# Kernel optimization log

Measured on AMD Instinct MI355X. Metric: run time of the kernel, lower is better.

Reference implementation:

```python
import jax, jax.numpy as jnp
import numpy as np

N_NODES = 100000
N_EDGES = 1600000
IN_CH = 128
OUT_CH = 64


def setup_inputs() -> dict:
    key = jax.random.key(0)
    k1, k2, k3 = jax.random.split(key, 3)
    x = jax.random.normal(k1, (N_NODES, IN_CH), dtype=jnp.float32)
    edge_index = jax.random.randint(k2, (2, N_EDGES), 0, N_NODES, dtype=jnp.int64)
    # Glorot-style init for the GCN weight, zero bias (PyG defaults)
    W = jax.random.normal(k3, (IN_CH, OUT_CH), dtype=jnp.float32) * (1.0 / np.sqrt(IN_CH))
    b = jnp.zeros((OUT_CH,), dtype=jnp.float32)
    return {"x": x, "edge_index": edge_index, "W": W, "b": b}


def reference(x, edge_index, W, b):
    n = x.shape[0]
    # add self loops (GCNConv default add_self_loops=True)
    loop = jnp.arange(n, dtype=edge_index.dtype)
    row = jnp.concatenate([edge_index[0], loop])  # source
    col = jnp.concatenate([edge_index[1], loop])  # target
    # symmetric degree normalization on augmented graph
    deg = jax.ops.segment_sum(jnp.ones_like(col, dtype=x.dtype), col, num_segments=n)
    dinv = jnp.where(deg > 0, jax.lax.rsqrt(deg), 0.0)
    norm = dinv[row] * dinv[col]  # [E+N]
    # linear transform first (out_channels < in_channels), then gather-scale-scatter
    h = x @ W  # [N, OUT]
    msgs = h[row] * norm[:, None]  # [E+N, OUT]
    out = jax.ops.segment_sum(msgs, col, num_segments=n)  # [N, OUT]
    return out + b
```

## Files before the change

kernel.cpp:

```cpp
#include <hip/hip_runtime.h>
#include <hip/hip_bf16.h>


#define IN_CH 128
#define OUT_CH 64
#define BSHIFT 7
#define BNODES 128
#define MAX_NB 800
#define CH_EDGES 7168
#define SORT_CAP 4096
#define XSTR 136

typedef short bf16x8 __attribute__((ext_vector_type(8)));
typedef float f32x4  __attribute__((ext_vector_type(4)));

__device__ __forceinline__ unsigned short f2b(float f) {
    unsigned int u = __float_as_uint(f);
    return (unsigned short)((u + 0x7FFFu + ((u >> 16) & 1u)) >> 16);
}

__global__ __launch_bounds__(256) void wprep_kernel(const float* __restrict__ W,
                                                    unsigned short* __restrict__ wbt) {
    int t = blockIdx.x * 256 + threadIdx.x;
    int k = t >> 6, nn = t & 63;
    wbt[nn * IN_CH + k] = f2b(W[t]);
}

__global__ __launch_bounds__(1024) void count_kernel(const int* __restrict__ col,
                                                     int* __restrict__ blkcnt,
                                                     int E, int NBLK, int NB) {
    __shared__ int h[MAX_NB];
    int tid = threadIdx.x;
    for (int i = tid; i < NB; i += 1024) h[i] = 0;
    __syncthreads();
    int e0 = blockIdx.x * CH_EDGES;
    #pragma unroll
    for (int r = 0; r < CH_EDGES / 1024; ++r) {
        int e = e0 + r * 1024 + tid;
        if (e < E) atomicAdd(&h[col[e] >> BSHIFT], 1);
    }
    __syncthreads();
    for (int i = tid; i < NB; i += 1024) blkcnt[i * NBLK + blockIdx.x] = h[i];
}

__global__ __launch_bounds__(256) void scan1_kernel(const int* __restrict__ v_in,
                                                    int* __restrict__ partial, int n) {
    __shared__ int s[256];
    int tid = threadIdx.x;
    int i   = blockIdx.x * 256 + tid;
    int v   = (i < n) ? v_in[i] : 0;
    s[tid] = v; __syncthreads();
    #pragma unroll
    for (int off = 1; off < 256; off <<= 1) {
        int t = (tid >= off) ? s[tid - off] : 0;
        __syncthreads();
        s[tid] += t;
        __syncthreads();
    }
    if (tid == 255) partial[blockIdx.x] = s[255];
}

__global__ __launch_bounds__(1024) void scan2_kernel(int* __restrict__ partial, int nb) {
    __shared__ int s[1024];
    int tid = threadIdx.x;
    int v   = (tid < nb) ? partial[tid] : 0;
    s[tid] = v; __syncthreads();
    #pragma unroll
    for (int off = 1; off < 1024; off <<= 1) {
        int t = (tid >= off) ? s[tid - off] : 0;
        __syncthreads();
        s[tid] += t;
        __syncthreads();
    }
    if (tid < nb) partial[tid] = s[tid] - v;
}

__global__ __launch_bounds__(256) void scan3_kernel(const int* __restrict__ v_in,
                                                    const int* __restrict__ partial,
                                                    int* __restrict__ v_out,
                                                    int* __restrict__ bucket_start,
                                                    int n, int NBLK, int NB, int E) {
    __shared__ int s[256];
    int tid = threadIdx.x;
    int i   = blockIdx.x * 256 + tid;
    int v   = (i < n) ? v_in[i] : 0;
    s[tid] = v; __syncthreads();
    #pragma unroll
    for (int off = 1; off < 256; off <<= 1) {
        int t = (tid >= off) ? s[tid - off] : 0;
        __syncthreads();
        s[tid] += t;
        __syncthreads();
    }
    if (i < n) {
        int excl = partial[blockIdx.x] + s[tid] - v;
        v_out[i] = excl;
        if (i % NBLK == 0) bucket_start[i / NBLK] = excl;
    }
    if (i == 0) bucket_start[NB] = E;
}

__global__ __launch_bounds__(1024) void place_kernel(const int* __restrict__ row,
                                                     const int* __restrict__ col,
                                                     const int* __restrict__ blkoff,
                                                     int* __restrict__ pairs,
                                                     int E, int NBLK, int NB) {
    __shared__ int cur[MAX_NB];
    int tid = threadIdx.x;
    for (int i = tid; i < NB; i += 1024) cur[i] = blkoff[i * NBLK + blockIdx.x];
    __syncthreads();
    int e0 = blockIdx.x * CH_EDGES;
    #pragma unroll
    for (int r2 = 0; r2 < CH_EDGES / 1024; ++r2) {
        int e = e0 + r2 * 1024 + tid;
        if (e < E) {
            int c = col[e];
            int b = c >> BSHIFT;
            int pos = atomicAdd(&cur[b], 1);
            pairs[pos] = row[e] | ((c & (BNODES - 1)) << 17);
        }
    }
}

__global__ __launch_bounds__(256) void bucket_sort_kernel(
    const int* __restrict__ bucket_start, const int* __restrict__ pairs,
    int* __restrict__ csr_row, int* __restrict__ row_start,
    float* __restrict__ dinv, int n, int E)
{
    __shared__ int cnt[BNODES];
    __shared__ int deg[BNODES];
    __shared__ int cur[BNODES];
    __shared__ int sorted[SORT_CAP];

    int b = blockIdx.x, tid = threadIdx.x;
    int node0 = b << BSHIFT;
    int nodeCnt = min(BNODES, n - node0);
    int s0 = bucket_start[b], s1 = bucket_start[b + 1];
    int m = s1 - s0;

    if (tid < BNODES) cnt[tid] = 0;
    __syncthreads();
    for (int e = s0 + tid; e < s1; e += 256) atomicAdd(&cnt[pairs[e] >> 17], 1);
    __syncthreads();
    if (tid < BNODES) deg[tid] = cnt[tid];
    __syncthreads();
    #pragma unroll
    for (int off = 1; off < BNODES; off <<= 1) {
        int t = (tid >= off && tid < BNODES) ? cnt[tid - off] : 0;
        __syncthreads();
        if (tid < BNODES) cnt[tid] += t;
        __syncthreads();
    }
    if (tid < BNODES) {
        int excl = cnt[tid] - deg[tid];
        cur[tid] = excl;
        if (tid < nodeCnt) {
            row_start[node0 + tid] = s0 + excl;
            dinv[node0 + tid] = rsqrtf((float)(deg[tid] + 1));
        }
    }
    if (b == gridDim.x - 1 && tid == 0) row_start[n] = E;
    __syncthreads();

    if (m <= SORT_CAP) {
        for (int e = s0 + tid; e < s1; e += 256) {
            int p   = pairs[e];
            int pos = atomicAdd(&cur[p >> 17], 1);
            sorted[pos] = p & 0x1FFFF;
        }
        __syncthreads();
        for (int i = tid; i < m; i += 256) csr_row[s0 + i] = sorted[i];
    } else {
        if (tid < BNODES) cur[tid] += s0;
        __syncthreads();
        for (int e = s0 + tid; e < s1; e += 256) {
            int p   = pairs[e];
            int pos = atomicAdd(&cur[p >> 17], 1);
            csr_row[pos] = p & 0x1FFFF;
        }
    }
}

__global__ __launch_bounds__(256) void gemm_kernel(
    const float* __restrict__ x, const unsigned short* __restrict__ wbt,
    const float* __restrict__ dinv, unsigned short* __restrict__ hpb, int n)
{
    __shared__ __align__(16) unsigned short xl[64 * XSTR];
    __shared__ __align__(16) unsigned short wl[64 * XSTR];

    int tid  = threadIdx.x;
    int row0 = blockIdx.x * 64;

    {
        const uint4* src = (const uint4*)wbt;
        #pragma unroll
        for (int i = 0; i < 4; ++i) {
            int flat = tid + i * 256;
            int nn = flat >> 4, c = flat & 15;
            *(uint4*)(wl + nn * XSTR + c * 8) = src[flat];
        }
    }
    #pragma unroll
    for (int i = 0; i < 4; ++i) {
        int r  = (tid >> 4) + i * 16;
        int c  = tid & 15;
        int gr = row0 + r;
        float4 v0 = make_float4(0.f,0.f,0.f,0.f), v1 = v0;
        float d = 0.f;
        if (gr < n) {
            d = dinv[gr];
            const float4* xr = (const float4*)(x + (size_t)gr * IN_CH);
            v0 = xr[c * 2]; v1 = xr[c * 2 + 1];
        }
        uint4 p;
        p.x = ((unsigned)f2b(v0.y * d) << 16) | f2b(v0.x * d);
        p.y = ((unsigned)f2b(v0.w * d) << 16) | f2b(v0.z * d);
        p.z = ((unsigned)f2b(v1.y * d) << 16) | f2b(v1.x * d);
        p.w = ((unsigned)f2b(v1.w * d) << 16) | f2b(v1.z * d);
        *(uint4*)(xl + r * XSTR + c * 8) = p;
    }
    __syncthreads();

    int lane = tid & 63, w = tid >> 6;
    int mrow = lane & 15;
    int g    = lane >> 4;

    f32x4 acc0 = {0,0,0,0}, acc1 = {0,0,0,0}, acc2 = {0,0,0,0}, acc3 = {0,0,0,0};
    const unsigned short* xbase = xl + (w * 16 + mrow) * XSTR + g * 8;
    const unsigned short* wbase = wl + mrow * XSTR + g * 8;

    #pragma unroll
    for (int k4 = 0; k4 < 4; ++k4) {
        bf16x8 a  = *(const bf16x8*)(xbase + k4 * 32);
        bf16x8 b0 = *(const bf16x8*)(wbase +             k4 * 32);
        bf16x8 b1 = *(const bf16x8*)(wbase + 16 * XSTR + k4 * 32);
        bf16x8 b2 = *(const bf16x8*)(wbase + 32 * XSTR + k4 * 32);
        bf16x8 b3 = *(const bf16x8*)(wbase + 48 * XSTR + k4 * 32);
        acc0 = __builtin_amdgcn_mfma_f32_16x16x32_bf16(a, b0, acc0, 0, 0, 0);
        acc1 = __builtin_amdgcn_mfma_f32_16x16x32_bf16(a, b1, acc1, 0, 0, 0);
        acc2 = __builtin_amdgcn_mfma_f32_16x16x32_bf16(a, b2, acc2, 0, 0, 0);
        acc3 = __builtin_amdgcn_mfma_f32_16x16x32_bf16(a, b3, acc3, 0, 0, 0);
    }
    __syncthreads();

    {
        int cm = g * 4;
        #pragma unroll
        for (int r = 0; r < 4; ++r) {
            unsigned short* crow = xl + (w * 16 + cm + r) * XSTR + mrow;
            crow[ 0] = f2b(acc0[r]);
            crow[16] = f2b(acc1[r]);
            crow[32] = f2b(acc2[r]);
            crow[48] = f2b(acc3[r]);
        }
    }
    __syncthreads();
    #pragma unroll
    for (int i = 0; i < 2; ++i) {
        int flat = tid + i * 256;
        int r = flat >> 3, c = flat & 7;
        int gr = row0 + r;
        if (gr < n) {
            uint4 v = *(const uint4*)(xl + r * XSTR + c * 8);
            *(uint4*)(hpb + (size_t)gr * OUT_CH + c * 8) = v;
        }
    }
}

__global__ __launch_bounds__(256) void aggregate_kernel(
    const int* __restrict__ row_start, const int* __restrict__ csr_row,
    const unsigned short* __restrict__ hpb, const float* __restrict__ dinv,
    const float* __restrict__ bias, float* __restrict__ out, int n)
{
    int wid  = (blockIdx.x * 256 + threadIdx.x) >> 6;
    int lane = threadIdx.x & 63;
    if (wid >= n) return;
    int half = lane >> 5;
    int hl   = lane & 31;

    const unsigned int* hp32 = (const unsigned int*)hpb;

    int s0 = row_start[wid];
    int s1 = row_start[wid + 1];

    float a0l=0.f,a0h=0.f,a1l=0.f,a1h=0.f,a2l=0.f,a2h=0.f,a3l=0.f,a3h=0.f;

    for (int base = s0; base < s1; base += 64) {
        int cnt  = min(64, s1 - base);
        int ridx = (base + lane < s1) ? csr_row[base + lane] : 0;
        int j = 0;
        for (; j + 8 <= cnt; j += 8) {
            int r0 = __shfl(ridx, j     + half);
            int r1 = __shfl(ridx, j + 2 + half);
            int r2 = __shfl(ridx, j + 4 + half);
            int r3 = __shfl(ridx, j + 6 + half);
            unsigned int v0 = hp32[(size_t)r0 * 32 + hl];
            unsigned int v1 = hp32[(size_t)r1 * 32 + hl];
            unsigned int v2 = hp32[(size_t)r2 * 32 + hl];
            unsigned int v3 = hp32[(size_t)r3 * 32 + hl];
            a0l += __uint_as_float(v0 << 16); a0h += __uint_as_float(v0 & 0xFFFF0000u);
            a1l += __uint_as_float(v1 << 16); a1h += __uint_as_float(v1 & 0xFFFF0000u);
            a2l += __uint_as_float(v2 << 16); a2h += __uint_as_float(v2 & 0xFFFF0000u);
            a3l += __uint_as_float(v3 << 16); a3h += __uint_as_float(v3 & 0xFFFF0000u);
        }
        for (; j < cnt; j += 2) {
            int e = j + half;
            int r = __shfl(ridx, e);
            unsigned int v = (e < cnt) ? hp32[(size_t)r * 32 + hl] : 0u;
            a0l += __uint_as_float(v << 16); a0h += __uint_as_float(v & 0xFFFF0000u);
        }
    }
    float sl = ((a0l + a1l) + (a2l + a3l));
    float sh = ((a0h + a1h) + (a2h + a3h));
    sl += __shfl_xor(sl, 32);
    sh += __shfl_xor(sh, 32);

    if (half == 0) {
        unsigned int sv = hp32[(size_t)wid * 32 + hl];
        sl += __uint_as_float(sv << 16);
        sh += __uint_as_float(sv & 0xFFFF0000u);
        float d = dinv[wid];
        float2 bb = ((const float2*)bias)[hl];
        float2 o;
        o.x = fmaf(d, sl, bb.x);
        o.y = fmaf(d, sh, bb.y);
        ((float2*)(out + (size_t)wid * OUT_CH))[hl] = o;
    }
}

extern "C" void kernel_launch(void* const* d_in, const int* in_sizes, int n_in,
                              void* d_out, int out_size, void* d_ws, size_t ws_size,
                              hipStream_t stream) {
    const float* x  = (const float*)d_in[0];
    const int*   ei = (const int*)d_in[1];
    const float* W  = (const float*)d_in[2];
    const float* b  = (const float*)d_in[3];
    float*       out = (float*)d_out;

    int n = in_sizes[0] / IN_CH;
    int E = in_sizes[1] / 2;
    const int* row = ei;
    const int* col = ei + E;

    int NB   = (n + BNODES - 1) >> BSHIFT;
    int NBLK = (E + CH_EDGES - 1) / CH_EDGES;
    int TOT  = NB * NBLK;
    int nbs  = (TOT + 255) / 256;

    char* ws = (char*)d_ws;
    int*   blkcnt       = (int*)ws;   ws += (size_t)TOT * 4;
    int*   blkoff       = (int*)ws;   ws += (size_t)TOT * 4;
    int*   partial      = (int*)ws;   ws += 1024 * 4;
    int*   bucket_start = (int*)ws;   ws += (size_t)(NB + 1) * 4;
    int*   row_start    = (int*)ws;   ws += (size_t)(n + 1) * 4;
    float* dinv         = (float*)ws; ws += (size_t)n * 4;
    int*   csr_row      = (int*)ws;   ws += (size_t)E * 4;
    unsigned short* wbt = (unsigned short*)ws; ws += (size_t)IN_CH * OUT_CH * 2;
    ws = (char*)(((uintptr_t)ws + 255) & ~(uintptr_t)255);
    int*            pairs = (int*)ws;
    unsigned short* hpb   = (unsigned short*)ws;

    wprep_kernel      <<<(IN_CH * OUT_CH) / 256, 256, 0, stream>>>(W, wbt);
    count_kernel      <<<NBLK, 1024, 0, stream>>>(col, blkcnt, E, NBLK, NB);
    scan1_kernel      <<<nbs, 256, 0, stream>>>(blkcnt, partial, TOT);
    scan2_kernel      <<<1, 1024, 0, stream>>>(partial, nbs);
    scan3_kernel      <<<nbs, 256, 0, stream>>>(blkcnt, partial, blkoff, bucket_start,
                                                TOT, NBLK, NB, E);
    place_kernel      <<<NBLK, 1024, 0, stream>>>(row, col, blkoff, pairs, E, NBLK, NB);
    bucket_sort_kernel<<<NB, 256, 0, stream>>>(bucket_start, pairs, csr_row, row_start, dinv, n, E);
    gemm_kernel       <<<(n + 63) / 64, 256, 0, stream>>>(x, wbt, dinv, hpb, n);
    aggregate_kernel  <<<(n + 3) / 4, 256, 0, stream>>>(row_start, csr_row, hpb, dinv, b, out, n);
}
```

Before: 185.9 us.

## Replace per-block count scan with global bucket atomics; widen aggregate unroll

Each count block now adds its local histogram straight into global per-bucket totals. A single-block scan then produces bucket starts and cursors, and place recounts its chunk locally before reserving ranges with one global atomic per bucket. This drops the blkcnt matrix and two scan kernels, trading them for a recount of col in place and a nondeterministic edge order within each bucket, which bucket_sort later sorts. The aggregate inner loop also moves to 16 edges per iteration with 8 independent accumulator pairs and predicated tails, for more memory-level parallelism.

```diff
diff --git a/kernel.cpp b/kernel.cpp
--- a/kernel.cpp
+++ b/kernel.cpp
@@ -20,15 +20,18 @@
 }
 
 __global__ __launch_bounds__(256) void wprep_kernel(const float* __restrict__ W,
-                                                    unsigned short* __restrict__ wbt) {
+                                                    unsigned short* __restrict__ wbt,
+                                                    int* __restrict__ bucket_cnt,
+                                                    int NB) {
     int t = blockIdx.x * 256 + threadIdx.x;
     int k = t >> 6, nn = t & 63;
     wbt[nn * IN_CH + k] = f2b(W[t]);
+    if (t < NB) bucket_cnt[t] = 0;
 }
 
 __global__ __launch_bounds__(1024) void count_kernel(const int* __restrict__ col,
-                                                     int* __restrict__ blkcnt,
-                                                     int E, int NBLK, int NB) {
+                                                     int* __restrict__ bucket_cnt,
+                                                     int E, int NB) {
     __shared__ int h[MAX_NB];
     int tid = threadIdx.x;
     for (int i = tid; i < NB; i += 1024) h[i] = 0;
@@ -40,30 +43,17 @@
         if (e < E) atomicAdd(&h[col[e] >> BSHIFT], 1);
     }
     __syncthreads();
-    for (int i = tid; i < NB; i += 1024) blkcnt[i * NBLK + blockIdx.x] = h[i];
-}
-
-__global__ __launch_bounds__(256) void scan1_kernel(const int* __restrict__ v_in,
-                                                    int* __restrict__ partial, int n) {
-    __shared__ int s[256];
-    int tid = threadIdx.x;
-    int i   = blockIdx.x * 256 + tid;
-    int v   = (i < n) ? v_in[i] : 0;
-    s[tid] = v; __syncthreads();
-    #pragma unroll
-    for (int off = 1; off < 256; off <<= 1) {
-        int t = (tid >= off) ? s[tid - off] : 0;
-        __syncthreads();
-        s[tid] += t;
-        __syncthreads();
-    }
-    if (tid == 255) partial[blockIdx.x] = s[255];
-}
-
-__global__ __launch_bounds__(1024) void scan2_kernel(int* __restrict__ partial, int nb) {
+    for (int i = tid; i < NB; i += 1024)
+        if (h[i]) atomicAdd(&bucket_cnt[i], h[i]);
+}
+
+__global__ __launch_bounds__(1024) void scanB_kernel(const int* __restrict__ bucket_cnt,
+                                                     int* __restrict__ bucket_start,
+                                                     int* __restrict__ cursor,
+                                                     int NB, int E) {
     __shared__ int s[1024];
     int tid = threadIdx.x;
-    int v   = (tid < nb) ? partial[tid] : 0;
+    int v   = (tid < NB) ? bucket_cnt[tid] : 0;
     s[tid] = v; __syncthreads();
     #pragma unroll
     for (int off = 1; off < 1024; off <<= 1) {
@@ -72,51 +62,42 @@
         s[tid] += t;
         __syncthreads();
     }
-    if (tid < nb) partial[tid] = s[tid] - v;
-}
-
-__global__ __launch_bounds__(256) void scan3_kernel(const int* __restrict__ v_in,
-                                                    const int* __restrict__ partial,
-                                                    int* __restrict__ v_out,
-                                                    int* __restrict__ bucket_start,
-                                                    int n, int NBLK, int NB, int E) {
-    __shared__ int s[256];
-    int tid = threadIdx.x;
-    int i   = blockIdx.x * 256 + tid;
-    int v   = (i < n) ? v_in[i] : 0;
-    s[tid] = v; __syncthreads();
-    #pragma unroll
-    for (int off = 1; off < 256; off <<= 1) {
-        int t = (tid >= off) ? s[tid - off] : 0;
-        __syncthreads();
-        s[tid] += t;
-        __syncthreads();
-    }
-    if (i < n) {
-        int excl = partial[blockIdx.x] + s[tid] - v;
-        v_out[i] = excl;
-        if (i % NBLK == 0) bucket_start[i / NBLK] = excl;
-    }
-    if (i == 0) bucket_start[NB] = E;
+    if (tid < NB) {
+        int excl = s[tid] - v;
+        bucket_start[tid] = excl;
+        cursor[tid] = excl;
+    }
+    if (tid == 0) bucket_start[NB] = E;
 }
 
 __global__ __launch_bounds__(1024) void place_kernel(const int* __restrict__ row,
                                                      const int* __restrict__ col,
-                                                     const int* __restrict__ blkoff,
+                                                     int* __restrict__ cursor,
                                                      int* __restrict__ pairs,
-                                                     int E, int NBLK, int NB) {
-    __shared__ int cur[MAX_NB];
+                                                     int E, int NB) {
+    __shared__ int h[MAX_NB];
     int tid = threadIdx.x;
-    for (int i = tid; i < NB; i += 1024) cur[i] = blkoff[i * NBLK + blockIdx.x];
+    for (int i = tid; i < NB; i += 1024) h[i] = 0;
     __syncthreads();
     int e0 = blockIdx.x * CH_EDGES;
+    #pragma unroll
+    for (int r1 = 0; r1 < CH_EDGES / 1024; ++r1) {
+        int e = e0 + r1 * 1024 + tid;
+        if (e < E) atomicAdd(&h[col[e] >> BSHIFT], 1);
+    }
+    __syncthreads();
+    for (int i = tid; i < NB; i += 1024) {
+        int c = h[i];
+        if (c) h[i] = atomicAdd(&cursor[i], c);
+    }
+    __syncthreads();
     #pragma unroll
     for (int r2 = 0; r2 < CH_EDGES / 1024; ++r2) {
         int e = e0 + r2 * 1024 + tid;
         if (e < E) {
             int c = col[e];
             int b = c >> BSHIFT;
-            int pos = atomicAdd(&cur[b], 1);
+            int pos = atomicAdd(&h[b], 1);
             pairs[pos] = row[e] | ((c & (BNODES - 1)) << 17);
         }
     }
@@ -283,35 +264,41 @@
     int s0 = row_start[wid];
     int s1 = row_start[wid + 1];
 
-    float a0l=0.f,a0h=0.f,a1l=0.f,a1h=0.f,a2l=0.f,a2h=0.f,a3l=0.f,a3h=0.f;
+    float al0=0.f,al1=0.f,al2=0.f,al3=0.f,al4=0.f,al5=0.f,al6=0.f,al7=0.f;
+    float ah0=0.f,ah1=0.f,ah2=0.f,ah3=0.f,ah4=0.f,ah5=0.f,ah6=0.f,ah7=0.f;
 
     for (int base = s0; base < s1; base += 64) {
         int cnt  = min(64, s1 - base);
         int ridx = (base + lane < s1) ? csr_row[base + lane] : 0;
-        int j = 0;
-        for (; j + 8 <= cnt; j += 8) {
-            int r0 = __shfl(ridx, j     + half);
-            int r1 = __shfl(ridx, j + 2 + half);
-            int r2 = __shfl(ridx, j + 4 + half);
-            int r3 = __shfl(ridx, j + 6 + half);
-            unsigned int v0 = hp32[(size_t)r0 * 32 + hl];
-            unsigned int v1 = hp32[(size_t)r1 * 32 + hl];
-            unsigned int v2 = hp32[(size_t)r2 * 32 + hl];
-            unsigned int v3 = hp32[(size_t)r3 * 32 + hl];
-            a0l += __uint_as_float(v0 << 16); a0h += __uint_as_float(v0 & 0xFFFF0000u);
-            a1l += __uint_as_float(v1 << 16); a1h += __uint_as_float(v1 & 0xFFFF0000u);
-            a2l += __uint_as_float(v2 << 16); a2h += __uint_as_float(v2 & 0xFFFF0000u);
-            a3l += __uint_as_float(v3 << 16); a3h += __uint_as_float(v3 & 0xFFFF0000u);
-        }
-        for (; j < cnt; j += 2) {
-            int e = j + half;
-            int r = __shfl(ridx, e);
-            unsigned int v = (e < cnt) ? hp32[(size_t)r * 32 + hl] : 0u;
-            a0l += __uint_as_float(v << 16); a0h += __uint_as_float(v & 0xFFFF0000u);
-        }
-    }
-    float sl = ((a0l + a1l) + (a2l + a3l));
-    float sh = ((a0h + a1h) + (a2h + a3h));
+        for (int j0 = 0; j0 < cnt; j0 += 16) {
+            int e0 = j0      + half, e1 = j0 +  2 + half;
+            int e2 = j0 +  4 + half, e3 = j0 +  6 + half;
+            int e4 = j0 +  8 + half, e5 = j0 + 10 + half;
+            int e6 = j0 + 12 + half, e7 = j0 + 14 + half;
+            int r0 = __shfl(ridx, e0), r1 = __shfl(ridx, e1);
+            int r2 = __shfl(ridx, e2), r3 = __shfl(ridx, e3);
+            int r4 = __shfl(ridx, e4), r5 = __shfl(ridx, e5);
+            int r6 = __shfl(ridx, e6), r7 = __shfl(ridx, e7);
+            unsigned v0 = (e0 < cnt) ? hp32[(size_t)r0 * 32 + hl] : 0u;
+            unsigned v1 = (e1 < cnt) ? hp32[(size_t)r1 * 32 + hl] : 0u;
+            unsigned v2 = (e2 < cnt) ? hp32[(size_t)r2 * 32 + hl] : 0u;
+            unsigned v3 = (e3 < cnt) ? hp32[(size_t)r3 * 32 + hl] : 0u;
+            unsigned v4 = (e4 < cnt) ? hp32[(size_t)r4 * 32 + hl] : 0u;
+            unsigned v5 = (e5 < cnt) ? hp32[(size_t)r5 * 32 + hl] : 0u;
+            unsigned v6 = (e6 < cnt) ? hp32[(size_t)r6 * 32 + hl] : 0u;
+            unsigned v7 = (e7 < cnt) ? hp32[(size_t)r7 * 32 + hl] : 0u;
+            al0 += __uint_as_float(v0 << 16); ah0 += __uint_as_float(v0 & 0xFFFF0000u);
+            al1 += __uint_as_float(v1 << 16); ah1 += __uint_as_float(v1 & 0xFFFF0000u);
+            al2 += __uint_as_float(v2 << 16); ah2 += __uint_as_float(v2 & 0xFFFF0000u);
+            al3 += __uint_as_float(v3 << 16); ah3 += __uint_as_float(v3 & 0xFFFF0000u);
+            al4 += __uint_as_float(v4 << 16); ah4 += __uint_as_float(v4 & 0xFFFF0000u);
+            al5 += __uint_as_float(v5 << 16); ah5 += __uint_as_float(v5 & 0xFFFF0000u);
+            al6 += __uint_as_float(v6 << 16); ah6 += __uint_as_float(v6 & 0xFFFF0000u);
+            al7 += __uint_as_float(v7 << 16); ah7 += __uint_as_float(v7 & 0xFFFF0000u);
+        }
+    }
+    float sl = ((al0 + al1) + (al2 + al3)) + ((al4 + al5) + (al6 + al7));
+    float sh = ((ah0 + ah1) + (ah2 + ah3)) + ((ah4 + ah5) + (ah6 + ah7));
     sl += __shfl_xor(sl, 32);
     sh += __shfl_xor(sh, 32);
 
@@ -344,14 +331,11 @@
 
     int NB   = (n + BNODES - 1) >> BSHIFT;
     int NBLK = (E + CH_EDGES - 1) / CH_EDGES;
-    int TOT  = NB * NBLK;
-    int nbs  = (TOT + 255) / 256;
 
     char* ws = (char*)d_ws;
-    int*   blkcnt       = (int*)ws;   ws += (size_t)TOT * 4;
-    int*   blkoff       = (int*)ws;   ws += (size_t)TOT * 4;
-    int*   partial      = (int*)ws;   ws += 1024 * 4;
+    int*   bucket_cnt   = (int*)ws;   ws += (size_t)NB * 4;
     int*   bucket_start = (int*)ws;   ws += (size_t)(NB + 1) * 4;
+    int*   cursor       = (int*)ws;   ws += (size_t)NB * 4;
     int*   row_start    = (int*)ws;   ws += (size_t)(n + 1) * 4;
     float* dinv         = (float*)ws; ws += (size_t)n * 4;
     int*   csr_row      = (int*)ws;   ws += (size_t)E * 4;
@@ -360,13 +344,10 @@
     int*            pairs = (int*)ws;
     unsigned short* hpb   = (unsigned short*)ws;
 
-    wprep_kernel      <<<(IN_CH * OUT_CH) / 256, 256, 0, stream>>>(W, wbt);
-    count_kernel      <<<NBLK, 1024, 0, stream>>>(col, blkcnt, E, NBLK, NB);
-    scan1_kernel      <<<nbs, 256, 0, stream>>>(blkcnt, partial, TOT);
-    scan2_kernel      <<<1, 1024, 0, stream>>>(partial, nbs);
-    scan3_kernel      <<<nbs, 256, 0, stream>>>(blkcnt, partial, blkoff, bucket_start,
-                                                TOT, NBLK, NB, E);
-    place_kernel      <<<NBLK, 1024, 0, stream>>>(row, col, blkoff, pairs, E, NBLK, NB);
+    wprep_kernel      <<<(IN_CH * OUT_CH) / 256, 256, 0, stream>>>(W, wbt, bucket_cnt, NB);
+    count_kernel      <<<NBLK, 1024, 0, stream>>>(col, bucket_cnt, E, NB);
+    scanB_kernel      <<<1, 1024, 0, stream>>>(bucket_cnt, bucket_start, cursor, NB, E);
+    place_kernel      <<<NBLK, 1024, 0, stream>>>(row, col, cursor, pairs, E, NB);
     bucket_sort_kernel<<<NB, 256, 0, stream>>>(bucket_start, pairs, csr_row, row_start, dinv, n, E);
     gemm_kernel       <<<(n + 63) / 64, 256, 0, stream>>>(x, wbt, dinv, hpb, n);
     aggregate_kernel  <<<(n + 3) / 4, 256, 0, stream>>>(row_start, csr_row, hpb, dinv, b, out, n);
```

New measurement: 181.2 us. -2.5%, faster.
